# Optimization experiments

Hardware: AMD Instinct MI355X
Metric: run time of the kernel (lower is better)

## Reference

```python
import jax, jax.numpy as jnp
import numpy as np
from jax import lax

NB_HEADS = 8
SR_RATIO = 4
LN_EPS = 1e-6


def layer_norm(x, g, b):
    mu = jnp.mean(x, axis=-1, keepdims=True)
    var = jnp.mean(jnp.square(x - mu), axis=-1, keepdims=True)
    return (x - mu) * lax.rsqrt(var + LN_EPS) * g + b


def setup_inputs() -> dict:
    key = jax.random.key(0)
    ks = jax.random.split(key, 6)
    B, H, W, C = 16, 64, 64, 256
    N = H * W
    s = 0.02
    return {
        "x": jax.random.normal(ks[0], (B, N, C), jnp.float32),
        "q_w": jax.random.normal(ks[1], (C, C), jnp.float32) * s,
        "q_b": jnp.zeros((C,), jnp.float32),
        "kv_w": jax.random.normal(ks[2], (C, 2 * C), jnp.float32) * s,
        "kv_b": jnp.zeros((2 * C,), jnp.float32),
        "sr_w": jax.random.normal(ks[3], (SR_RATIO, SR_RATIO, C, C), jnp.float32) * s,
        "sr_b": jnp.zeros((C,), jnp.float32),
        "norm_g": jnp.ones((C,), jnp.float32),
        "norm_b": jnp.zeros((C,), jnp.float32),
        "proj_w": jax.random.normal(ks[4], (C, C), jnp.float32) * s,
        "proj_b": jnp.zeros((C,), jnp.float32),
        "grid_h": H,
        "grid_w": W,
    }


def reference(x, q_w, q_b, kv_w, kv_b, sr_w, sr_b, norm_g, norm_b, proj_w, proj_b, grid_h, grid_w):
    B, N, C = x.shape
    hd = C // NB_HEADS
    scale = hd ** (-0.5)

    # query projection -> [B, nh, N, hd]
    q = (x @ q_w + q_b).reshape(B, N, NB_HEADS, hd).transpose(0, 2, 1, 3)

    # spatial reduction: conv stride=kernel=sr_ratio on NHWC grid
    xg = x.reshape(B, grid_h, grid_w, C)
    xs = lax.conv_general_dilated(
        xg, sr_w, window_strides=(SR_RATIO, SR_RATIO), padding="VALID",
        dimension_numbers=("NHWC", "HWIO", "NHWC")) + sr_b
    M = (grid_h // SR_RATIO) * (grid_w // SR_RATIO)
    xs = layer_norm(xs.reshape(B, M, C), norm_g, norm_b)

    # key/value projection -> [B, nh, M, hd] each
    kv = (xs @ kv_w + kv_b).reshape(B, M, 2, NB_HEADS, hd).transpose(2, 0, 3, 1, 4)
    k, v = kv[0], kv[1]

    attn = jax.nn.softmax(scale * jnp.einsum("bhnd,bhmd->bhnm", q, k), axis=-1)
    out = jnp.einsum("bhnm,bhmd->bhnd", attn, v)  # [B, nh, N, hd]
    out = out.transpose(0, 2, 1, 3).reshape(B, N, C)
    return out @ proj_w + proj_b
```

## Files before the change

### kernel.cpp

```cpp
#include <hip/hip_runtime.h>
#include <math.h>

#define B_   16
#define CC   256
#define NN   4096
#define MM   256
#define NH   8
#define HD   32
#define QSCALE (0.17677669529663687f * 1.4426950408889634f)

typedef float fx4 __attribute__((ext_vector_type(4)));
typedef short sx4 __attribute__((ext_vector_type(4)));
typedef short sx8 __attribute__((ext_vector_type(8)));

__device__ inline short f2bf(float f) {
  unsigned u = __builtin_bit_cast(unsigned, f);
  u += 0x7FFFu + ((u >> 16) & 1u);
  return (short)(u >> 16);
}
__device__ inline float bf2f(short s) {
  unsigned u = ((unsigned)(unsigned short)s) << 16;
  return __builtin_bit_cast(float, u);
}
__device__ inline unsigned cvtpk_bf16(float a, float b) {
  unsigned r;
  asm("v_cvt_pk_bf16_f32 %0, %1, %2" : "=v"(r) : "v"(a), "v"(b));
  return r;
}
__device__ inline float fexp2(float x) {
#if __has_builtin(__builtin_amdgcn_exp2f)
  return __builtin_amdgcn_exp2f(x);
#else
  return exp2f(x);
#endif
}
__device__ inline float frcp(float x) {
#if __has_builtin(__builtin_amdgcn_rcpf)
  return __builtin_amdgcn_rcpf(x);
#else
  return 1.0f / x;
#endif
}

template<bool KT>
__global__ __launch_bounds__(256) void wsplit_kernel(
    const float* __restrict__ W, short* __restrict__ Th, short* __restrict__ Tl,
    int K, int N)
{
  __shared__ float Tile[64][65];
  const int t = threadIdx.x;
  const int k0 = blockIdx.y << 6, n0 = blockIdx.x << 6;
#pragma unroll
  for (int i = 0; i < 4; ++i) {
    int idx = t + (i << 8);
    int k = idx >> 4, n4 = (idx & 15) << 2;
    float4 v = *(const float4*)&W[(size_t)(k0 + k) * N + n0 + n4];
    Tile[k][n4 + 0] = v.x; Tile[k][n4 + 1] = v.y;
    Tile[k][n4 + 2] = v.z; Tile[k][n4 + 3] = v.w;
  }
  __syncthreads();
#pragma unroll
  for (int i = 0; i < 4; ++i) {
    int idx = t + (i << 8);
    int n = idx >> 4, k4 = (idx & 15) << 2;
    sx4 h, lo;
#pragma unroll
    for (int j = 0; j < 4; ++j) {
      float v = Tile[k4 + j][n];
      short hh = f2bf(v);
      h[j] = hh;
      lo[j] = f2bf(v - bf2f(hh));
    }
    int kk = k0 + k4, nn = n0 + n;
    size_t dst;
    if constexpr (KT)
      dst = ((size_t)(kk >> 5) * N << 5) + ((size_t)nn << 5) + (kk & 31);
    else
      dst = (size_t)nn * K + kk;
    *(sx4*)&Th[dst] = h;
    *(sx4*)&Tl[dst] = lo;
  }
}

template<int AM, int EP>
__global__ __launch_bounds__(256) void gemm_wide_kernel(
    const void* __restrict__ Av, const short* __restrict__ Alo,
    const short* __restrict__ Bth, const short* __restrict__ Btl,
    const float* __restrict__ bias, float* __restrict__ C,
    short* __restrict__ qout, int M, int K)
{
  __shared__ short Bhs[256][36];
  __shared__ short Bls[256][36];
  const int t = threadIdx.x;
  const int bm = blockIdx.x << 6;
  const int w = t >> 6, l = t & 63, g = l >> 4, c = l & 15;
  const int g8 = g << 3;
  const int arow = bm + (w << 4) + c;
  const int srow = t >> 2;
  const int skc  = (t & 3) << 3;

  sx8 pb0h, pb1h, pb2h, pb3h, pb0l, pb1l, pb2l, pb3l;
  auto LOADB = [&](int k0) {
    const size_t tb = ((size_t)(k0 >> 5) << 13) + ((size_t)t << 3);
    pb0h = *(const sx8*)&Bth[tb];         pb1h = *(const sx8*)&Bth[tb + 2048];
    pb2h = *(const sx8*)&Bth[tb + 4096];  pb3h = *(const sx8*)&Bth[tb + 6144];
    pb0l = *(const sx8*)&Btl[tb];         pb1l = *(const sx8*)&Btl[tb + 2048];
    pb2l = *(const sx8*)&Btl[tb + 4096];  pb3l = *(const sx8*)&Btl[tb + 6144];
  };

  float4 pa0, pa1; sx8 pah, pal;
  auto LOADA = [&](int k0) {
    if constexpr (AM == 2) {
      size_t idx = ((size_t)(arow >> 12) << 20) + ((size_t)(k0 >> 5) << 17)
                 + ((size_t)(arow & 4095) << 5) + g8;
      pah = *(const sx8*)&((const short*)Av)[idx];
      pal = *(const sx8*)&Alo[idx];
    } else {
      const float* ap = (const float*)Av + (size_t)arow * K + k0 + g8;
      pa0 = *(const float4*)ap;
      pa1 = *(const float4*)(ap + 4);
    }
  };

  fx4 acc[16];
#pragma unroll
  for (int j = 0; j < 16; ++j) acc[j] = fx4{0.f, 0.f, 0.f, 0.f};

  LOADB(0); LOADA(0);
  for (int k0 = 0; k0 < K; k0 += 32) {
    *(sx8*)&Bhs[srow][skc]       = pb0h;
    *(sx8*)&Bhs[64 + srow][skc]  = pb1h;
    *(sx8*)&Bhs[128 + srow][skc] = pb2h;
    *(sx8*)&Bhs[192 + srow][skc] = pb3h;
    *(sx8*)&Bls[srow][skc]       = pb0l;
    *(sx8*)&Bls[64 + srow][skc]  = pb1l;
    *(sx8*)&Bls[128 + srow][skc] = pb2l;
    *(sx8*)&Bls[192 + srow][skc] = pb3l;
    sx8 ah, al;
    if constexpr (AM == 2) { ah = pah; al = pal; }
    else {
      ah[0]=f2bf(pa0.x); al[0]=f2bf(pa0.x-bf2f(ah[0]));
      ah[1]=f2bf(pa0.y); al[1]=f2bf(pa0.y-bf2f(ah[1]));
      ah[2]=f2bf(pa0.z); al[2]=f2bf(pa0.z-bf2f(ah[2]));
      ah[3]=f2bf(pa0.w); al[3]=f2bf(pa0.w-bf2f(ah[3]));
      ah[4]=f2bf(pa1.x); al[4]=f2bf(pa1.x-bf2f(ah[4]));
      ah[5]=f2bf(pa1.y); al[5]=f2bf(pa1.y-bf2f(ah[5]));
      ah[6]=f2bf(pa1.z); al[6]=f2bf(pa1.z-bf2f(ah[6]));
      ah[7]=f2bf(pa1.w); al[7]=f2bf(pa1.w-bf2f(ah[7]));
    }
    __syncthreads();
    if (k0 + 32 < K) { LOADB(k0 + 32); LOADA(k0 + 32); }
#pragma unroll
    for (int j = 0; j < 16; ++j) {
      sx8 bh = *(const sx8*)&Bhs[(j << 4) + c][g8];
      sx8 bl = *(const sx8*)&Bls[(j << 4) + c][g8];
      acc[j] = __builtin_amdgcn_mfma_f32_16x16x32_bf16(ah, bh, acc[j], 0, 0, 0);
      acc[j] = __builtin_amdgcn_mfma_f32_16x16x32_bf16(al, bh, acc[j], 0, 0, 0);
      acc[j] = __builtin_amdgcn_mfma_f32_16x16x32_bf16(ah, bl, acc[j], 0, 0, 0);
    }
    __syncthreads();
  }

  const int orow = bm + (w << 4) + (g << 2);
#pragma unroll
  for (int j = 0; j < 16; ++j) {
    const int col = (j << 4) + c;
    const float bb = bias[col];
    if constexpr (EP == 0) {
#pragma unroll
      for (int i = 0; i < 4; ++i)
        C[(size_t)(orow + i) * 256 + col] = acc[j][i] + bb;
    } else {
      const int h = col >> 5, d = col & 31;
#pragma unroll
      for (int i = 0; i < 4; ++i) {
        int r = orow + i;
        qout[((size_t)(((r >> 12) << 3) + h) * 4096 + (r & 4095)) * 32 + d]
            = f2bf((acc[j][i] + bb) * QSCALE);
      }
    }
  }
}

template<bool GATHER, int EPI>
__global__ __launch_bounds__(256) void gemm_split_kernel(
    const float* __restrict__ A, const short* __restrict__ Bth,
    const short* __restrict__ Btl, const float* __restrict__ bias,
    float* __restrict__ C, short* __restrict__ kout, short* __restrict__ vout,
    int M, int N, int K)
{
  __shared__ short Ah[64][40], Al[64][40], Bh[64][40], Bl[64][40];
  const int t = threadIdx.x;
  const int bm = blockIdx.y << 6, bn = blockIdx.x << 6;
  const int ar = t >> 2, ak = (t & 3) << 3;
  const int bc = t >> 2, bk = (t & 3) << 3;

  int sp_base = 0;
  if (GATHER) {
    int gr = bm + ar;
    int b = gr >> 8, mm2 = gr & 255;
    int oh = mm2 >> 4, ow = mm2 & 15;
    sp_base = b * 4096 + oh * 256 + ow * 4;
  }
  const size_t brow = (size_t)(bn + bc) * K;

  const int KS = K / gridDim.z;
  const int kbeg = blockIdx.z * KS, kend = kbeg + KS;

  float4 pa0, pa1; sx8 pbh, pbl;
  auto LOADG = [&](int k0) {
    int k = k0 + ak;
    const float* ap;
    if (GATHER) {
      int pos = k >> 8, ci = k & 255;
      ap = &A[(size_t)(sp_base + ((pos >> 2) << 6) + (pos & 3)) * 256 + ci];
    } else {
      ap = &A[(size_t)(bm + ar) * K + k];
    }
    pa0 = *(const float4*)ap;
    pa1 = *(const float4*)(ap + 4);
    pbh = *(const sx8*)&Bth[brow + k0 + bk];
    pbl = *(const sx8*)&Btl[brow + k0 + bk];
  };

  const int w = t >> 6, l = t & 63, g = l >> 4, c = l & 15;
  const int wr = w >> 1, wc = w & 1;
  const int ra0 = (wr << 5) + c, ra1 = ra0 + 16;
  const int cb0 = (wc << 5) + c, cb1 = cb0 + 16;
  const int g8 = g << 3;

  fx4 acc00 = {0.f,0.f,0.f,0.f}, acc01 = acc00, acc10 = acc00, acc11 = acc00;

  LOADG(kbeg);
  for (int k0 = kbeg; k0 < kend; k0 += 32) {
    sx4 AH0, AL0, AH1, AL1;
    AH0[0]=f2bf(pa0.x); AL0[0]=f2bf(pa0.x-bf2f(AH0[0]));
    AH0[1]=f2bf(pa0.y); AL0[1]=f2bf(pa0.y-bf2f(AH0[1]));
    AH0[2]=f2bf(pa0.z); AL0[2]=f2bf(pa0.z-bf2f(AH0[2]));
    AH0[3]=f2bf(pa0.w); AL0[3]=f2bf(pa0.w-bf2f(AH0[3]));
    AH1[0]=f2bf(pa1.x); AL1[0]=f2bf(pa1.x-bf2f(AH1[0]));
    AH1[1]=f2bf(pa1.y); AL1[1]=f2bf(pa1.y-bf2f(AH1[1]));
    AH1[2]=f2bf(pa1.z); AL1[2]=f2bf(pa1.z-bf2f(AH1[2]));
    AH1[3]=f2bf(pa1.w); AL1[3]=f2bf(pa1.w-bf2f(AH1[3]));
    *(sx4*)&Ah[ar][ak]     = AH0;  *(sx4*)&Ah[ar][ak + 4] = AH1;
    *(sx4*)&Al[ar][ak]     = AL0;  *(sx4*)&Al[ar][ak + 4] = AL1;
    *(sx8*)&Bh[bc][bk] = pbh;      *(sx8*)&Bl[bc][bk] = pbl;
    __syncthreads();
    if (k0 + 32 < kend) LOADG(k0 + 32);

    sx8 a0h = *(const sx8*)&Ah[ra0][g8];
    sx8 a0l = *(const sx8*)&Al[ra0][g8];
    sx8 a1h = *(const sx8*)&Ah[ra1][g8];
    sx8 a1l = *(const sx8*)&Al[ra1][g8];
    sx8 b0h = *(const sx8*)&Bh[cb0][g8];
    sx8 b0l = *(const sx8*)&Bl[cb0][g8];
    sx8 b1h = *(const sx8*)&Bh[cb1][g8];
    sx8 b1l = *(const sx8*)&Bl[cb1][g8];

    acc00 = __builtin_amdgcn_mfma_f32_16x16x32_bf16(a0h, b0h, acc00, 0, 0, 0);
    acc01 = __builtin_amdgcn_mfma_f32_16x16x32_bf16(a0h, b1h, acc01, 0, 0, 0);
    acc10 = __builtin_amdgcn_mfma_f32_16x16x32_bf16(a1h, b0h, acc10, 0, 0, 0);
    acc11 = __builtin_amdgcn_mfma_f32_16x16x32_bf16(a1h, b1h, acc11, 0, 0, 0);
    acc00 = __builtin_amdgcn_mfma_f32_16x16x32_bf16(a0l, b0h, acc00, 0, 0, 0);
    acc01 = __builtin_amdgcn_mfma_f32_16x16x32_bf16(a0l, b1h, acc01, 0, 0, 0);
    acc10 = __builtin_amdgcn_mfma_f32_16x16x32_bf16(a1l, b0h, acc10, 0, 0, 0);
    acc11 = __builtin_amdgcn_mfma_f32_16x16x32_bf16(a1l, b1h, acc11, 0, 0, 0);
    acc00 = __builtin_amdgcn_mfma_f32_16x16x32_bf16(a0h, b0l, acc00, 0, 0, 0);
    acc01 = __builtin_amdgcn_mfma_f32_16x16x32_bf16(a0h, b1l, acc01, 0, 0, 0);
    acc10 = __builtin_amdgcn_mfma_f32_16x16x32_bf16(a1h, b0l, acc10, 0, 0, 0);
    acc11 = __builtin_amdgcn_mfma_f32_16x16x32_bf16(a1h, b1l, acc11, 0, 0, 0);
    __syncthreads();
  }

  const int col0 = bn + (wc << 5);
  const int row0 = bm + (wr << 5) + (g << 2);
  if constexpr (EPI == 1) {
    float* Cz = C + (size_t)blockIdx.z * M * N;
#pragma unroll
    for (int i = 0; i < 4; ++i) {
      Cz[(size_t)(row0 + i) * N + col0 + c]           = acc00[i];
      Cz[(size_t)(row0 + i) * N + col0 + 16 + c]      = acc01[i];
      Cz[(size_t)(row0 + 16 + i) * N + col0 + c]      = acc10[i];
      Cz[(size_t)(row0 + 16 + i) * N + col0 + 16 + c] = acc11[i];
    }
  } else {
    const float b0 = bias[col0 + c], b1 = bias[col0 + 16 + c];
    auto emit = [&](int row, int n, float v) {
      int b = row >> 8, m = row & 255;
      short* dst = (n < 256) ? kout : vout;
      int nn = n & 255;
      int h = nn >> 5, d = nn & 31;
      dst[(size_t)(((b << 3) + h) * 256 + m) * 32 + d] = f2bf(v);
    };
#pragma unroll
    for (int i = 0; i < 4; ++i) {
      emit(row0 + i,      col0 + c,      acc00[i] + b0);
      emit(row0 + i,      col0 + 16 + c, acc01[i] + b1);
      emit(row0 + 16 + i, col0 + c,      acc10[i] + b0);
      emit(row0 + 16 + i, col0 + 16 + c, acc11[i] + b1);
    }
  }
}

__global__ __launch_bounds__(256) void ln_reduce_kernel(
    const float* __restrict__ parts, const float* __restrict__ bias,
    const float* __restrict__ g, const float* __restrict__ bta,
    float* __restrict__ xs)
{
  const int row = blockIdx.x, t = threadIdx.x;
  const size_t MN = (size_t)4096 * 256;
  const size_t off = (size_t)row * CC + t;
  float v = bias[t];
#pragma unroll
  for (int p = 0; p < 8; ++p) v += parts[p * MN + off];
  float s = v, s2 = v * v;
#pragma unroll
  for (int offs = 32; offs; offs >>= 1) {
    s  += __shfl_xor(s,  offs, 64);
    s2 += __shfl_xor(s2, offs, 64);
  }
  __shared__ float red[8];
  const int w = t >> 6, lane = t & 63;
  if (lane == 0) { red[w] = s; red[4 + w] = s2; }
  __syncthreads();
  float ts  = red[0] + red[1] + red[2] + red[3];
  float ts2 = red[4] + red[5] + red[6] + red[7];
  float mu  = ts * (1.0f / 256.0f);
  float var = ts2 * (1.0f / 256.0f) - mu * mu;
  float o = (v - mu) * rsqrtf(var + 1e-6f) * g[t] + bta[t];
  xs[off] = o;
}

__global__ __launch_bounds__(256, 3) void attn_mfma4_kernel(
    short* __restrict__ qob, short* __restrict__ olo,
    const short* __restrict__ kbf, const short* __restrict__ vbf)
{
  __shared__ short Vt[32 * 264];
  __shared__ short Ps[4 * 16 * 264];

  const int tid = threadIdx.x;
  const int bid = blockIdx.x;
  const int nt = bid & 63, h = (bid >> 6) & 7, b = bid >> 9;
  const int n0 = nt << 6;
  const int bh = (b << 3) + h;
  const short* kb = kbf + (size_t)bh * 8192;
  const short* vb = vbf + (size_t)bh * 8192;

  {
    const int msrc = ((tid & 15) << 4) | (tid >> 4);
    sx8 v0 = *(const sx8*)&vb[msrc * 32 + 0];
    sx8 v1 = *(const sx8*)&vb[msrc * 32 + 8];
    sx8 v2 = *(const sx8*)&vb[msrc * 32 + 16];
    sx8 v3 = *(const sx8*)&vb[msrc * 32 + 24];
#pragma unroll
    for (int e = 0; e < 8; ++e) {
      Vt[(e)      * 264 + tid] = v0[e];
      Vt[(8 + e)  * 264 + tid] = v1[e];
      Vt[(16 + e) * 264 + tid] = v2[e];
      Vt[(24 + e) * 264 + tid] = v3[e];
    }
  }

  const int w = tid >> 6, l = tid & 63;
  const int g = l >> 4, c = l & 15;

  sx8 aq = *(const sx8*)&qob[((size_t)bh * 4096 + n0 + w * 16 + c) * 32 + (g << 3)];

  fx4 acc[16];
#pragma unroll
  for (int j = 0; j < 16; ++j) {
    sx8 bk = *(const sx8*)&kb[(j * 16 + c) * 32 + (g << 3)];
    fx4 z = {0.f, 0.f, 0.f, 0.f};
    acc[j] = __builtin_amdgcn_mfma_f32_16x16x32_bf16(aq, bk, z, 0, 0, 0);
  }

  float mx[4], sm[4];
#pragma unroll
  for (int i = 0; i < 4; ++i) {
    float m0 = acc[0][i];
#pragma unroll
    for (int j = 1; j < 16; ++j) m0 = fmaxf(m0, acc[j][i]);
    m0 = fmaxf(m0, __shfl_xor(m0, 1, 64));
    m0 = fmaxf(m0, __shfl_xor(m0, 2, 64));
    m0 = fmaxf(m0, __shfl_xor(m0, 4, 64));
    m0 = fmaxf(m0, __shfl_xor(m0, 8, 64));
    mx[i] = m0;
  }
#pragma unroll
  for (int i = 0; i < 4; ++i) {
    float s0 = 0.f;
#pragma unroll
    for (int j = 0; j < 16; ++j) {
      float p = fexp2(acc[j][i] - mx[i]);
      acc[j][i] = p; s0 += p;
    }
    s0 += __shfl_xor(s0, 1, 64);
    s0 += __shfl_xor(s0, 2, 64);
    s0 += __shfl_xor(s0, 4, 64);
    s0 += __shfl_xor(s0, 8, 64);
    sm[i] = s0;
  }

  const int pbase = (w << 4) * 264;
#pragma unroll
  for (int i = 0; i < 4; ++i) {
    unsigned p0 = cvtpk_bf16(acc[0][i],  acc[1][i]);
    unsigned p1 = cvtpk_bf16(acc[2][i],  acc[3][i]);
    unsigned p2 = cvtpk_bf16(acc[4][i],  acc[5][i]);
    unsigned p3 = cvtpk_bf16(acc[6][i],  acc[7][i]);
    unsigned p4 = cvtpk_bf16(acc[8][i],  acc[9][i]);
    unsigned p5 = cvtpk_bf16(acc[10][i], acc[11][i]);
    unsigned p6 = cvtpk_bf16(acc[12][i], acc[13][i]);
    unsigned p7 = cvtpk_bf16(acc[14][i], acc[15][i]);
    unsigned* dst = (unsigned*)&Ps[pbase + ((g << 2) + i) * 264 + (c << 4)];
    uint4 lo4; lo4.x = p0; lo4.y = p1; lo4.z = p2; lo4.w = p3;
    uint4 hi4; hi4.x = p4; hi4.y = p5; hi4.z = p6; hi4.w = p7;
    *(uint4*)dst       = lo4;
    *(uint4*)(dst + 4) = hi4;
  }

  __syncthreads();

  fx4 o0 = {0.f,0.f,0.f,0.f}, o1 = {0.f,0.f,0.f,0.f};
#pragma unroll
  for (int s = 0; s < 8; ++s) {
    sx8 ap  = *(const sx8*)&Ps[pbase + c * 264 + (s << 5) + (g << 3)];
    sx8 bv0 = *(const sx8*)&Vt[(c)      * 264 + (s << 5) + (g << 3)];
    sx8 bv1 = *(const sx8*)&Vt[(16 + c) * 264 + (s << 5) + (g << 3)];
    o0 = __builtin_amdgcn_mfma_f32_16x16x32_bf16(ap, bv0, o0, 0, 0, 0);
    o1 = __builtin_amdgcn_mfma_f32_16x16x32_bf16(ap, bv1, o1, 0, 0, 0);
  }

#pragma unroll
  for (int i = 0; i < 4; ++i) {
    float inv = frcp(sm[i]);
    int n = n0 + w * 16 + (g << 2) + i;
    size_t base = ((size_t)bh * 4096 + n) * 32;
    float v0 = o0[i] * inv, v1 = o1[i] * inv;
    short h0 = f2bf(v0), h1 = f2bf(v1);
    qob[base + c]      = h0;  olo[base + c]      = f2bf(v0 - bf2f(h0));
    qob[base + 16 + c] = h1;  olo[base + 16 + c] = f2bf(v1 - bf2f(h1));
  }
}

extern "C" void kernel_launch(void* const* d_in, const int* in_sizes, int n_in,
                              void* d_out, int out_size, void* d_ws, size_t ws_size,
                              hipStream_t stream) {
  const float* x      = (const float*)d_in[0];
  const float* q_w    = (const float*)d_in[1];
  const float* q_b    = (const float*)d_in[2];
  const float* kv_w   = (const float*)d_in[3];
  const float* kv_b   = (const float*)d_in[4];
  const float* sr_w   = (const float*)d_in[5];
  const float* sr_b   = (const float*)d_in[6];
  const float* norm_g = (const float*)d_in[7];
  const float* norm_b = (const float*)d_in[8];
  const float* proj_w = (const float*)d_in[9];
  const float* proj_b = (const float*)d_in[10];
  float* out = (float*)d_out;

  float* xsbuf = (float*)d_ws;
  short* qbf   = (short*)(xsbuf + 1048576);
  short* olo   = qbf + 16777216;
  short* kbf   = olo + 16777216;
  short* vbf   = kbf + 2097152;
  short* qwt_h  = vbf + 2097152;
  short* qwt_l  = qwt_h + 65536;
  short* kvwt_h = qwt_l + 65536;
  short* kvwt_l = kvwt_h + 131072;
  short* pwt_h  = kvwt_l + 131072;
  short* pwt_l  = pwt_h + 65536;
  short* swt_h  = pwt_l + 65536;
  short* swt_l  = swt_h + 1048576;
  float* partf = out;

  dim3 blk(256);

  wsplit_kernel<true><<<dim3(CC/64, CC/64), blk, 0, stream>>>(q_w, qwt_h, qwt_l, CC, CC);
  wsplit_kernel<false><<<dim3(2*CC/64, CC/64), blk, 0, stream>>>(kv_w, kvwt_h, kvwt_l, CC, 2*CC);
  wsplit_kernel<true><<<dim3(CC/64, CC/64), blk, 0, stream>>>(proj_w, pwt_h, pwt_l, CC, CC);
  wsplit_kernel<false><<<dim3(CC/64, 4096/64), blk, 0, stream>>>(sr_w, swt_h, swt_l, 4096, CC);

  gemm_wide_kernel<0,3><<<dim3((B_*NN)/64), blk, 0, stream>>>(
      x, nullptr, qwt_h, qwt_l, q_b, nullptr, qbf, B_*NN, CC);

  gemm_split_kernel<true,1><<<dim3(CC/64, (B_*MM)/64, 8), blk, 0, stream>>>(
      x, swt_h, swt_l, sr_b, partf, nullptr, nullptr, B_*MM, CC, 4096);

  ln_reduce_kernel<<<B_ * MM, blk, 0, stream>>>(partf, sr_b, norm_g, norm_b, xsbuf);

  gemm_split_kernel<false,2><<<dim3((2*CC)/64, (B_*MM)/64, 1), blk, 0, stream>>>(
      xsbuf, kvwt_h, kvwt_l, kv_b, nullptr, kbf, vbf, B_*MM, 2*CC, CC);

  attn_mfma4_kernel<<<B_ * NH * (NN / 64), blk, 0, stream>>>(qbf, olo, kbf, vbf);

  gemm_wide_kernel<2,0><<<dim3((B_*NN)/64), blk, 0, stream>>>(
      qbf, olo, pwt_h, pwt_l, proj_b, out, nullptr, B_*NN, CC);
}
```

Baseline: 226.8 us.

## Emit V pre-transposed from KV GEMM and read it directly from global in attention

The KV projection epilogue now writes V in a transposed, permuted [bh][d][m] layout, so the attention kernel no longer stages and transposes V through shared memory. This removes the Vt LDS buffer and one block barrier, and the launch-bounds occupancy hint rises from 3 to 4. In exchange, the V operands of the PV MFMA loop come straight from global/L2 with strided rows, and the GEMM epilogue now does scattered 2-byte stores for V.

```diff
diff --git a/kernel.cpp b/kernel.cpp
--- a/kernel.cpp
+++ b/kernel.cpp
@@ -287,10 +287,14 @@
     const float b0 = bias[col0 + c], b1 = bias[col0 + 16 + c];
     auto emit = [&](int row, int n, float v) {
       int b = row >> 8, m = row & 255;
-      short* dst = (n < 256) ? kout : vout;
       int nn = n & 255;
       int h = nn >> 5, d = nn & 31;
-      dst[(size_t)(((b << 3) + h) * 256 + m) * 32 + d] = f2bf(v);
+      if (n < 256) {
+        kout[(size_t)(((b << 3) + h) * 256 + m) * 32 + d] = f2bf(v);
+      } else {
+        int mp = ((m & 15) << 4) | (m >> 4);
+        vout[((size_t)(((b << 3) + h) * 32 + d)) * 256 + mp] = f2bf(v);
+      }
     };
 #pragma unroll
     for (int i = 0; i < 4; ++i) {
@@ -331,11 +335,10 @@
   xs[off] = o;
 }
 
-__global__ __launch_bounds__(256, 3) void attn_mfma4_kernel(
+__global__ __launch_bounds__(256, 4) void attn_mfma7_kernel(
     short* __restrict__ qob, short* __restrict__ olo,
-    const short* __restrict__ kbf, const short* __restrict__ vbf)
+    const short* __restrict__ kbf, const short* __restrict__ vtp)
 {
-  __shared__ short Vt[32 * 264];
   __shared__ short Ps[4 * 16 * 264];
 
   const int tid = threadIdx.x;
@@ -344,22 +347,7 @@
   const int n0 = nt << 6;
   const int bh = (b << 3) + h;
   const short* kb = kbf + (size_t)bh * 8192;
-  const short* vb = vbf + (size_t)bh * 8192;
-
-  {
-    const int msrc = ((tid & 15) << 4) | (tid >> 4);
-    sx8 v0 = *(const sx8*)&vb[msrc * 32 + 0];
-    sx8 v1 = *(const sx8*)&vb[msrc * 32 + 8];
-    sx8 v2 = *(const sx8*)&vb[msrc * 32 + 16];
-    sx8 v3 = *(const sx8*)&vb[msrc * 32 + 24];
-#pragma unroll
-    for (int e = 0; e < 8; ++e) {
-      Vt[(e)      * 264 + tid] = v0[e];
-      Vt[(8 + e)  * 264 + tid] = v1[e];
-      Vt[(16 + e) * 264 + tid] = v2[e];
-      Vt[(24 + e) * 264 + tid] = v3[e];
-    }
-  }
+  const short* vt = vtp + (size_t)bh * 8192;
 
   const int w = tid >> 6, l = tid & 63;
   const int g = l >> 4, c = l & 15;
@@ -419,14 +407,12 @@
     *(uint4*)(dst + 4) = hi4;
   }
 
-  __syncthreads();
-
   fx4 o0 = {0.f,0.f,0.f,0.f}, o1 = {0.f,0.f,0.f,0.f};
 #pragma unroll
   for (int s = 0; s < 8; ++s) {
     sx8 ap  = *(const sx8*)&Ps[pbase + c * 264 + (s << 5) + (g << 3)];
-    sx8 bv0 = *(const sx8*)&Vt[(c)      * 264 + (s << 5) + (g << 3)];
-    sx8 bv1 = *(const sx8*)&Vt[(16 + c) * 264 + (s << 5) + (g << 3)];
+    sx8 bv0 = *(const sx8*)&vt[(size_t)(c)      * 256 + (s << 5) + (g << 3)];
+    sx8 bv1 = *(const sx8*)&vt[(size_t)(16 + c) * 256 + (s << 5) + (g << 3)];
     o0 = __builtin_amdgcn_mfma_f32_16x16x32_bf16(ap, bv0, o0, 0, 0, 0);
     o1 = __builtin_amdgcn_mfma_f32_16x16x32_bf16(ap, bv1, o1, 0, 0, 0);
   }
@@ -463,8 +449,8 @@
   short* qbf   = (short*)(xsbuf + 1048576);
   short* olo   = qbf + 16777216;
   short* kbf   = olo + 16777216;
-  short* vbf   = kbf + 2097152;
-  short* qwt_h  = vbf + 2097152;
+  short* vtp   = kbf + 2097152;
+  short* qwt_h  = vtp + 2097152;
   short* qwt_l  = qwt_h + 65536;
   short* kvwt_h = qwt_l + 65536;
   short* kvwt_l = kvwt_h + 131072;
@@ -490,9 +476,9 @@
   ln_reduce_kernel<<<B_ * MM, blk, 0, stream>>>(partf, sr_b, norm_g, norm_b, xsbuf);
 
   gemm_split_kernel<false,2><<<dim3((2*CC)/64, (B_*MM)/64, 1), blk, 0, stream>>>(
-      xsbuf, kvwt_h, kvwt_l, kv_b, nullptr, kbf, vbf, B_*MM, 2*CC, CC);
-
-  attn_mfma4_kernel<<<B_ * NH * (NN / 64), blk, 0, stream>>>(qbf, olo, kbf, vbf);
+      xsbuf, kvwt_h, kvwt_l, kv_b, nullptr, kbf, vtp, B_*MM, 2*CC, CC);
+
+  attn_mfma7_kernel<<<B_ * NH * (NN / 64), blk, 0, stream>>>(qbf, olo, kbf, vtp);
 
   gemm_wide_kernel<2,0><<<dim3((B_*NN)/64), blk, 0, stream>>>(
       qbf, olo, pwt_h, pwt_l, proj_b, out, nullptr, B_*NN, CC);
```

New measurement: 265.0 us. +16.9%, slower.
